# Optimization experiments

Hardware: AMD Instinct MI355X
Metric: run time of the kernel (lower is better)

Reference implementation:

```python
import jax, jax.numpy as jnp
import numpy as np

MEM_HEAD = 4
K_DIM = 256
HALF = K_DIM // 2          # 128
SUB_SIZE = 512
MEM_SIZE = SUB_SIZE * SUB_SIZE  # 262144
KNN = 32
HIDDEN = 512
BN_EPS = 1e-5


def setup_inputs() -> dict:
    key = jax.random.key(0)
    ks = jax.random.split(key, 9)
    B = 4096
    x = jax.random.normal(ks[0], (B, HIDDEN), jnp.float32)
    W1 = jax.random.normal(ks[1], (HIDDEN // 2, HIDDEN), jnp.float32) * (1.0 / np.sqrt(HIDDEN))
    b1 = jnp.zeros((HIDDEN // 2,), jnp.float32)
    W2 = jax.random.normal(ks[2], (2 * HIDDEN, HIDDEN // 2), jnp.float32) * (1.0 / np.sqrt(HIDDEN // 2))
    b2 = jnp.zeros((2 * HIDDEN,), jnp.float32)
    gamma = jnp.ones((2 * HIDDEN,), jnp.float32)
    beta = jnp.zeros((2 * HIDDEN,), jnp.float32)
    # product keys: (heads, 2 halves, n_sub_keys, half_dim), gaussian init
    keys = jax.random.normal(ks[3], (MEM_HEAD, 2, SUB_SIZE, HALF), jnp.float32)
    # EmbeddingBag value table, init std = HIDDEN^-0.5
    values = jax.random.normal(ks[4], (MEM_SIZE, HIDDEN), jnp.float32) * (HIDDEN ** -0.5)
    return dict(x=x, W1=W1, b1=b1, W2=W2, b2=b2, gamma=gamma, beta=beta, keys=keys, values=values)


def reference(x, W1, b1, W2, b2, gamma, beta, keys, values):
    B = x.shape[0]
    # QueryMLP: Linear -> ELU -> Linear -> BatchNorm1d (training-mode batch stats)
    h = jax.nn.elu(x @ W1.T + b1)
    h = h @ W2.T + b2                                  # (B, 2H)
    mu = h.mean(axis=0)
    var = h.var(axis=0)                                # biased, as torch BN
    h = (h - mu) * jax.lax.rsqrt(var + BN_EPS) * gamma + beta
    q = h.reshape(B, MEM_HEAD, K_DIM)                  # (B, heads, k_dim)
    q1, q2 = q[..., :HALF], q[..., HALF:]
    # sub-key scoring per head half
    s1 = jnp.einsum('bhd,hkd->bhk', q1, keys[:, 0])    # (B, heads, SUB_SIZE)
    s2 = jnp.einsum('bhd,hkd->bhk', q2, keys[:, 1])
    t1, i1 = jax.lax.top_k(s1, KNN)                    # (B, heads, KNN)
    t2, i2 = jax.lax.top_k(s2, KNN)
    # cartesian product of the two knn sets
    all_s = (t1[..., :, None] + t2[..., None, :]).reshape(B, MEM_HEAD, KNN * KNN)
    all_i = (i1[..., :, None] * SUB_SIZE + i2[..., None, :]).reshape(B, MEM_HEAD, KNN * KNN)
    sc, best = jax.lax.top_k(all_s, KNN)               # (B, heads, KNN)
    idx = jnp.take_along_axis(all_i, best, axis=-1)
    # softmax over KNN per (sample, head), as in the torch code (dim=-1 on (bs*head, KNN))
    w = jax.nn.softmax(sc, axis=-1).reshape(B, MEM_HEAD * KNN)
    idx = idx.reshape(B, MEM_HEAD * KNN)
    # weighted EmbeddingBag sum
    rows = values[idx]                                 # (B, heads*KNN, HIDDEN)
    out = jnp.einsum('bk,bkd->bd', w, rows)            # (B, HIDDEN)
    return out
```

## Files before the change

kernel.cpp:

```cpp
#include <hip/hip_runtime.h>
#include <math.h>

#define NROWS 4096
#define HIDN  512
#define H1N   256
#define H2N   1024
#define NHEAD 4
#define KDIM  256
#define HALFD 128
#define SUBS  512
#define KNN   32

typedef _Float16 f16x8 __attribute__((ext_vector_type(8)));
typedef _Float16 f16x4v __attribute__((ext_vector_type(4)));
typedef float f32x4  __attribute__((ext_vector_type(4)));

template<int C>
__device__ __forceinline__ unsigned dpp_umax(unsigned x) {
    unsigned m = (unsigned)__builtin_amdgcn_update_dpp((int)x, (int)x, C, 0xf, 0xf, false);
    return x > m ? x : m;
}
__device__ __forceinline__ unsigned wave_umax_bcast(unsigned x) {
    x = dpp_umax<0x111>(x);
    x = dpp_umax<0x112>(x);
    x = dpp_umax<0x114>(x);
    x = dpp_umax<0x118>(x);
    x = dpp_umax<0x142>(x);
    x = dpp_umax<0x143>(x);
    return (unsigned)__builtin_amdgcn_readlane((int)x, 63);
}
template<int C>
__device__ __forceinline__ float dpp_fadd(float x) {
    int m = __builtin_amdgcn_update_dpp(0, __float_as_int(x), C, 0xf, 0xf, true);
    return x + __int_as_float(m);
}
__device__ __forceinline__ float wave_fsum_bcast(float x) {
    x = dpp_fadd<0x111>(x);
    x = dpp_fadd<0x112>(x);
    x = dpp_fadd<0x114>(x);
    x = dpp_fadd<0x118>(x);
    x = dpp_fadd<0x142>(x);
    x = dpp_fadd<0x143>(x);
    return __int_as_float(__builtin_amdgcn_readlane(__float_as_int(x), 63));
}

template<int IB>
__device__ __forceinline__ unsigned pack_key(float v, int j) {
    unsigned b = __float_as_uint(v);
    unsigned x = (unsigned)((int)b >> 31) | 0x80000000u;
    unsigned k = b ^ x;
    constexpr unsigned LM = (1u << IB) - 1u;
    return (k & ~LM) | (LM - (unsigned)j);
}
template<int IB>
__device__ __forceinline__ float dec_key(unsigned k) {
    constexpr unsigned LM = (1u << IB) - 1u;
    unsigned kv = k & ~LM;
    unsigned x = (~(unsigned)((int)kv >> 31)) | 0x80000000u;
    return __uint_as_float(kv ^ x);
}

__device__ __forceinline__ void slot_to_ij(int s, int& io, int& jo) {
    constexpr int O[32] = {0,32,48,58,66,72,77,81,85,88,91,93,95,97,99,101,
                           103,104,105,106,107,108,109,110,111,112,113,114,115,116,117,118};
    int ii = 0, oo = 0;
    #pragma unroll
    for (int k = 1; k < 32; ++k) {
        bool ge = (s >= O[k]);
        ii += ge ? 1 : 0;
        oo = ge ? O[k] : oo;
    }
    io = ii; jo = s - oo;
}

__global__ __launch_bounds__(256)
void cvt_f16(const float* __restrict__ in, _Float16* __restrict__ out)
{
    int i = (blockIdx.x * 256 + threadIdx.x) * 4;
    float4 v = *(const float4*)&in[i];
    f16x4v o = {(_Float16)v.x, (_Float16)v.y, (_Float16)v.z, (_Float16)v.w};
    *(f16x4v*)&out[i] = o;
}

template<int BN, int ACT>
__global__ __launch_bounds__(256)
void gemm_f16(const _Float16* __restrict__ A, const _Float16* __restrict__ B,
              const float* __restrict__ bias, _Float16* __restrict__ C,
              int K, int lda, int ldb, int ldc)
{
    constexpr int WR = (BN == 128) ? 2 : 4;
    constexpr int WM = 128 / WR;
    constexpr int MT = WM / 16;
    constexpr int NT = 4;

    __shared__ _Float16 As[128 * 64];
    __shared__ _Float16 Bs[BN * 64];

    const int t    = threadIdx.x;
    const int m0   = blockIdx.x * 128, n0 = blockIdx.y * BN;
    const int lane = t & 63, wv = t >> 6;
    const int wr   = (BN == 128) ? (wv >> 1) : wv;
    const int wc   = (BN == 128) ? (wv & 1) : 0;
    const int sr   = t >> 3;
    const int sce  = (t & 7) * 8;
    const int swz  = sce * 2;

    const f32x4 fz = {0.f, 0.f, 0.f, 0.f};
    f32x4 acc[MT][NT];
    #pragma unroll
    for (int mt = 0; mt < MT; ++mt)
        #pragma unroll
        for (int nt = 0; nt < NT; ++nt) acc[mt][nt] = fz;

    for (int kb = 0; kb < K; kb += 64) {
        #pragma unroll
        for (int i = 0; i < 4; ++i) {
            int r = sr + 32 * i;
            uint4 v = *(const uint4*)&A[(size_t)(m0 + r) * lda + kb + sce];
            *(uint4*)((char*)As + r * 128 + (swz ^ ((r & 7) << 4))) = v;
        }
        #pragma unroll
        for (int i = 0; i < BN / 32; ++i) {
            int r = sr + 32 * i;
            uint4 v = *(const uint4*)&B[(size_t)(n0 + r) * ldb + kb + sce];
            *(uint4*)((char*)Bs + r * 128 + (swz ^ ((r & 7) << 4))) = v;
        }
        __syncthreads();
        #pragma unroll
        for (int ks = 0; ks < 2; ++ks) {
            const int kbyte = ks * 64 + (lane >> 4) * 16;
            f16x8 ah[MT], bf[NT];
            #pragma unroll
            for (int mt = 0; mt < MT; ++mt) {
                int r = wr * WM + mt * 16 + (lane & 15);
                ah[mt] = *(const f16x8*)((const char*)As + r * 128 + (kbyte ^ ((r & 7) << 4)));
            }
            #pragma unroll
            for (int nt = 0; nt < NT; ++nt) {
                int r = wc * 64 + nt * 16 + (lane & 15);
                bf[nt] = *(const f16x8*)((const char*)Bs + r * 128 + (kbyte ^ ((r & 7) << 4)));
            }
            #pragma unroll
            for (int mt = 0; mt < MT; ++mt)
                #pragma unroll
                for (int nt = 0; nt < NT; ++nt)
                    acc[mt][nt] = __builtin_amdgcn_mfma_f32_16x16x32_f16(ah[mt], bf[nt], acc[mt][nt], 0, 0, 0);
        }
        __syncthreads();
    }

    #pragma unroll
    for (int mt = 0; mt < MT; ++mt) {
        #pragma unroll
        for (int nt = 0; nt < NT; ++nt) {
            int col = n0 + wc * 64 + nt * 16 + (lane & 15);
            float bz = bias[col];
            #pragma unroll
            for (int j = 0; j < 4; ++j) {
                int row = m0 + wr * WM + mt * 16 + (lane >> 4) * 4 + j;
                float v = acc[mt][nt][j] + bz;
                if (ACT) v = v > 0.f ? v : expm1f(v);
                C[(size_t)row * ldc + col] = (_Float16)v;
            }
        }
    }
}

__global__ __launch_bounds__(256)
void bn_partial_h(const _Float16* __restrict__ h2f, float* __restrict__ part)
{
    int col = blockIdx.x * 256 + threadIdx.x;
    int r0  = blockIdx.y * 256;
    float s = 0.f, q = 0.f;
    for (int rr = r0; rr < r0 + 256; ++rr) {
        float v = (float)h2f[(size_t)rr * H2N + col];
        s += v; q += v * v;
    }
    part[(size_t)blockIdx.y * H2N + col] = s;
    part[(size_t)16 * H2N + (size_t)blockIdx.y * H2N + col] = q;
}

__global__ __launch_bounds__(256)
void bn_finalize(const float* __restrict__ part, const float* __restrict__ gamma,
                 const float* __restrict__ beta, float* __restrict__ scale,
                 float* __restrict__ shift)
{
    int col = blockIdx.x * 256 + threadIdx.x;
    float s = 0.f, q = 0.f;
    for (int c = 0; c < 16; ++c) {
        s += part[(size_t)c * H2N + col];
        q += part[(size_t)16 * H2N + (size_t)c * H2N + col];
    }
    float mu  = s * (1.f / NROWS);
    float var = q * (1.f / NROWS) - mu * mu;
    float sc  = gamma[col] / sqrtf(var + 1e-5f);
    scale[col] = sc;
    shift[col] = beta[col] - mu * sc;
}

__global__ __launch_bounds__(256)
void keys_prep(const float* __restrict__ keys, const float* __restrict__ scale,
               const float* __restrict__ shift, _Float16* __restrict__ keysp,
               float* __restrict__ biasp)
{
    const int gid  = blockIdx.x * 4 + (threadIdx.x >> 6);
    const int lane = threadIdx.x & 63;
    const int z    = gid >> 9;
    const float* krow = keys + (size_t)gid * HALFD;
    const int d0 = lane * 2;
    float k0 = krow[d0], k1 = krow[d0 + 1];
    float sc0 = scale[z * HALFD + d0], sc1 = scale[z * HALFD + d0 + 1];
    float sh0 = shift[z * HALFD + d0], sh1 = shift[z * HALFD + d0 + 1];
    _Float16 p0 = (_Float16)(sc0 * k0), p1 = (_Float16)(sc1 * k1);
    unsigned u;
    {
        union { _Float16 h[2]; unsigned u; } cvt;
        cvt.h[0] = p0; cvt.h[1] = p1;
        u = cvt.u;
    }
    *(unsigned*)&keysp[(size_t)gid * HALFD + d0] = u;
    float dot = wave_fsum_bcast(k0 * sh0 + k1 * sh1);
    if (lane == 0) biasp[gid] = dot;
}

__global__ __launch_bounds__(256)
void score_f16(const _Float16* __restrict__ h2f, const _Float16* __restrict__ keysp,
               const float* __restrict__ biasp, float* __restrict__ s1, float* __restrict__ s2)
{
    __shared__ _Float16 As[128 * 64];
    __shared__ _Float16 Bs[128 * 64];

    const int t    = threadIdx.x;
    const int z    = blockIdx.z;
    const int m0   = blockIdx.x * 128, n0 = blockIdx.y * 128;
    const int lane = t & 63, wv = t >> 6;
    const int wr   = wv >> 1, wc = wv & 1;
    const int sr   = t >> 3;
    const int sce  = (t & 7) * 8;
    const int swz  = sce * 2;

    const _Float16* A = h2f + z * HALFD;
    const _Float16* B = keysp + (size_t)z * SUBS * HALFD;
    float* outb = (z & 1) ? s2 : s1;
    const int hd = z >> 1;

    const f32x4 fz = {0.f, 0.f, 0.f, 0.f};
    f32x4 acc[4][4];
    #pragma unroll
    for (int mt = 0; mt < 4; ++mt)
        #pragma unroll
        for (int nt = 0; nt < 4; ++nt) acc[mt][nt] = fz;

    for (int kb = 0; kb < HALFD; kb += 64) {
        #pragma unroll
        for (int i = 0; i < 4; ++i) {
            int r = sr + 32 * i;
            uint4 v = *(const uint4*)&A[(size_t)(m0 + r) * H2N + kb + sce];
            *(uint4*)((char*)As + r * 128 + (swz ^ ((r & 7) << 4))) = v;
        }
        #pragma unroll
        for (int i = 0; i < 4; ++i) {
            int r = sr + 32 * i;
            uint4 v = *(const uint4*)&B[(size_t)(n0 + r) * HALFD + kb + sce];
            *(uint4*)((char*)Bs + r * 128 + (swz ^ ((r & 7) << 4))) = v;
        }
        __syncthreads();
        #pragma unroll
        for (int ks = 0; ks < 2; ++ks) {
            const int kbyte = ks * 64 + (lane >> 4) * 16;
            f16x8 af[4], bf[4];
            #pragma unroll
            for (int mt = 0; mt < 4; ++mt) {
                int r = wr * 64 + mt * 16 + (lane & 15);
                af[mt] = *(const f16x8*)((const char*)As + r * 128 + (kbyte ^ ((r & 7) << 4)));
            }
            #pragma unroll
            for (int nt = 0; nt < 4; ++nt) {
                int r = wc * 64 + nt * 16 + (lane & 15);
                bf[nt] = *(const f16x8*)((const char*)Bs + r * 128 + (kbyte ^ ((r & 7) << 4)));
            }
            #pragma unroll
            for (int mt = 0; mt < 4; ++mt)
                #pragma unroll
                for (int nt = 0; nt < 4; ++nt)
                    acc[mt][nt] = __builtin_amdgcn_mfma_f32_16x16x32_f16(af[mt], bf[nt], acc[mt][nt], 0, 0, 0);
        }
        __syncthreads();
    }

    #pragma unroll
    for (int mt = 0; mt < 4; ++mt) {
        #pragma unroll
        for (int nt = 0; nt < 4; ++nt) {
            int col = n0 + wc * 64 + nt * 16 + (lane & 15);
            float bz = biasp[z * SUBS + col];
            #pragma unroll
            for (int j = 0; j < 4; ++j) {
                int row = m0 + wr * 64 + mt * 16 + (lane >> 4) * 4 + j;
                outb[((size_t)row * NHEAD + hd) * SUBS + col] = acc[mt][nt][j] + bz;
            }
        }
    }
}

__global__ __launch_bounds__(512)
void topk_gather(const float* __restrict__ s1, const float* __restrict__ s2,
                 const float* __restrict__ values, float* __restrict__ out)
{
    const int b    = blockIdx.x;
    const int t    = threadIdx.x;
    const int w    = t >> 6;
    const int lane = t & 63;

    __shared__ unsigned Ksh[8][KNN];
    __shared__ float wgt_sh[NHEAD * KNN];
    __shared__ int   idx_sh[NHEAD * KNN];
    __shared__ float4 pacc[4][128];

    {
        const int head = w >> 1, half = w & 1;
        const float* srow = (half ? s2 : s1) + ((size_t)b * NHEAD + head) * SUBS;
        float4 va = ((const float4*)srow)[lane * 2];
        float4 vb = ((const float4*)srow)[lane * 2 + 1];
        const int j0 = lane * 8;
        unsigned k0 = pack_key<9>(va.x, j0+0), k1 = pack_key<9>(va.y, j0+1);
        unsigned k2 = pack_key<9>(va.z, j0+2), k3 = pack_key<9>(va.w, j0+3);
        unsigned k4 = pack_key<9>(vb.x, j0+4), k5 = pack_key<9>(vb.y, j0+5);
        unsigned k6 = pack_key<9>(vb.z, j0+6), k7 = pack_key<9>(vb.w, j0+7);

        #define CEU(a,b) { unsigned _mx = (a)>(b)?(a):(b); unsigned _mn = (a)>(b)?(b):(a); (a)=_mx; (b)=_mn; }
        CEU(k0,k1) CEU(k2,k3) CEU(k4,k5) CEU(k6,k7)
        CEU(k0,k2) CEU(k1,k3) CEU(k4,k6) CEU(k5,k7)
        CEU(k1,k2) CEU(k5,k6)
        CEU(k0,k4) CEU(k1,k5) CEU(k2,k6) CEU(k3,k7)
        CEU(k2,k4) CEU(k3,k5)
        CEU(k1,k2) CEU(k3,k4) CEU(k5,k6)
        #undef CEU

        unsigned kk = 0;
        #pragma unroll
        for (int rr = 0; rr < KNN; ++rr) {
            unsigned bv = wave_umax_bcast(k0);
            bool win = (k0 == bv);
            k0 = win ? k1 : k0;
            k1 = win ? k2 : k1;
            k2 = win ? k3 : k2;
            k3 = win ? k4 : k3;
            k4 = win ? k5 : k4;
            k5 = win ? k6 : k5;
            k6 = win ? k7 : k6;
            k7 = win ? 0u : k7;
            kk = (lane == rr) ? bv : kk;
        }
        if (lane < KNN) Ksh[w][lane] = kk;
    }
    __syncthreads();

    if (w < NHEAD) {
        const int h = w;
        const unsigned* T1 = Ksh[2*h];
        const unsigned* T2 = Ksh[2*h+1];

        unsigned c0 = 0, c1 = 0;
        {
            int ia, ja;
            slot_to_ij(lane, ia, ja);
            if (lane < 119) {
                float s = dec_key<9>(T1[ia]) + dec_key<9>(T2[ja]);
                c0 = pack_key<7>(s, lane);
            }
            if (lane + 64 < 119) {
                int ib2, jb2;
                slot_to_ij(lane + 64, ib2, jb2);
                float s = dec_key<9>(T1[ib2]) + dec_key<9>(T2[jb2]);
                c1 = pack_key<7>(s, lane + 64);
            }
        }

        unsigned kk = 0;
        #pragma unroll
        for (int rr = 0; rr < KNN; ++rr) {
            unsigned m  = c0 > c1 ? c0 : c1;
            unsigned bv = wave_umax_bcast(m);
            bool f0 = (c0 == bv);
            bool f1 = (c1 == bv);
            c0 = f0 ? 0u : c0;
            c1 = f1 ? 0u : c1;
            kk = (lane == rr) ? bv : kk;
        }

        unsigned mk = (unsigned)__builtin_amdgcn_readlane((int)kk, 0);
        float mx = dec_key<7>(mk);
        float sv = dec_key<7>(kk);
        float e  = (lane < KNN) ? __expf(sv - mx) : 0.f;
        float Z  = wave_fsum_bcast(e);

        if (lane < KNN) {
            int slot = 127 - (int)(kk & 127u);
            int i, j;
            slot_to_ij(slot, i, j);
            int i1 = 511 - (int)(T1[i] & 511u);
            int i2 = 511 - (int)(T2[j] & 511u);
            wgt_sh[h * KNN + lane] = e / Z;
            idx_sh[h * KNN + lane] = i1 * SUBS + i2;
        }
    }
    __syncthreads();

    const int sub = t >> 7;
    const int c4  = t & 127;
    #define EADDR(i) ((const float4*)(values + (size_t)idx_sh[((i)<<2)|sub] * HIDN) + c4)
    float4 b0 = *EADDR(0), b1 = *EADDR(1), b2 = *EADDR(2), b3 = *EADDR(3);
    float4 b4 = *EADDR(4), b5 = *EADDR(5), b6 = *EADDR(6), b7 = *EADDR(7);
    float4 a0 = make_float4(0.f,0.f,0.f,0.f);
    float4 a1 = make_float4(0.f,0.f,0.f,0.f);
    #define FMA4(acc, wg, v) { acc.x = fmaf(wg, v.x, acc.x); acc.y = fmaf(wg, v.y, acc.y); \
                               acc.z = fmaf(wg, v.z, acc.z); acc.w = fmaf(wg, v.w, acc.w); }
    #define STEPR(bi, ei, acc) { float wg = wgt_sh[((ei)<<2)|sub]; FMA4(acc, wg, bi); bi = *EADDR((ei)+8); }
    #define STEPN(bi, ei, acc) { float wg = wgt_sh[((ei)<<2)|sub]; FMA4(acc, wg, bi); }
    STEPR(b0, 0, a0) STEPR(b1, 1, a1) STEPR(b2, 2, a0) STEPR(b3, 3, a1)
    STEPR(b4, 4, a0) STEPR(b5, 5, a1) STEPR(b6, 6, a0) STEPR(b7, 7, a1)
    STEPR(b0, 8, a0) STEPR(b1, 9, a1) STEPR(b2,10, a0) STEPR(b3,11, a1)
    STEPR(b4,12, a0) STEPR(b5,13, a1) STEPR(b6,14, a0) STEPR(b7,15, a1)
    STEPR(b0,16, a0) STEPR(b1,17, a1) STEPR(b2,18, a0) STEPR(b3,19, a1)
    STEPR(b4,20, a0) STEPR(b5,21, a1) STEPR(b6,22, a0) STEPR(b7,23, a1)
    STEPN(b0,24, a0) STEPN(b1,25, a1) STEPN(b2,26, a0) STEPN(b3,27, a1)
    STEPN(b4,28, a0) STEPN(b5,29, a1) STEPN(b6,30, a0) STEPN(b7,31, a1)
    #undef STEPR
    #undef STEPN
    #undef FMA4
    #undef EADDR
    float4 acc;
    acc.x = a0.x + a1.x; acc.y = a0.y + a1.y;
    acc.z = a0.z + a1.z; acc.w = a0.w + a1.w;

    pacc[sub][c4] = acc;
    __syncthreads();
    if (t < 128) {
        float4 r0 = pacc[0][t], r1 = pacc[1][t], r2 = pacc[2][t], r3 = pacc[3][t];
        float4 r;
        r.x = (r0.x + r1.x) + (r2.x + r3.x);
        r.y = (r0.y + r1.y) + (r2.y + r3.y);
        r.z = (r0.z + r1.z) + (r2.z + r3.z);
        r.w = (r0.w + r1.w) + (r2.w + r3.w);
        ((float4*)(out + (size_t)b * HIDN))[t] = r;
    }
}

extern "C" void kernel_launch(void* const* d_in, const int* in_sizes, int n_in,
                              void* d_out, int out_size, void* d_ws, size_t ws_size,
                              hipStream_t stream)
{
    const float* x      = (const float*)d_in[0];
    const float* W1     = (const float*)d_in[1];
    const float* b1     = (const float*)d_in[2];
    const float* W2     = (const float*)d_in[3];
    const float* b2     = (const float*)d_in[4];
    const float* gamma  = (const float*)d_in[5];
    const float* beta   = (const float*)d_in[6];
    const float* keys   = (const float*)d_in[7];
    const float* values = (const float*)d_in[8];
    float* out = (float*)d_out;

    float* ws    = (float*)d_ws;
    float* part  = ws;
    float* scale = part + (size_t)32 * H2N;
    float* shift = scale + H2N;
    float* s1    = shift + H2N;
    float* s2    = s1 + (size_t)NROWS * NHEAD * SUBS;
    float* biasp = s2 + (size_t)NROWS * NHEAD * SUBS;
    _Float16* xh    = (_Float16*)(biasp + 4096);
    _Float16* w1h   = xh  + (size_t)NROWS * HIDN;
    _Float16* w2h   = w1h + (size_t)H1N * HIDN;
    _Float16* h1h   = w2h + (size_t)H2N * H1N;
    _Float16* h2f   = h1h + (size_t)NROWS * H1N;
    _Float16* keysp = h2f + (size_t)NROWS * H2N;

    cvt_f16<<<dim3((NROWS * HIDN) / 1024), 256, 0, stream>>>(x, xh);
    cvt_f16<<<dim3((H1N * HIDN) / 1024), 256, 0, stream>>>(W1, w1h);
    cvt_f16<<<dim3((H2N * H1N) / 1024), 256, 0, stream>>>(W2, w2h);

    gemm_f16<64, 1><<<dim3(NROWS/128, H1N/64), 256, 0, stream>>>(
        xh, w1h, b1, h1h, HIDN, HIDN, HIDN, H1N);
    gemm_f16<128, 0><<<dim3(NROWS/128, H2N/128), 256, 0, stream>>>(
        h1h, w2h, b2, h2f, H1N, H1N, H1N, H2N);

    bn_partial_h<<<dim3(H2N/256, 16), 256, 0, stream>>>(h2f, part);
    bn_finalize<<<dim3(H2N/256), 256, 0, stream>>>(part, gamma, beta, scale, shift);

    keys_prep<<<dim3(1024), 256, 0, stream>>>(keys, scale, shift, keysp, biasp);

    score_f16<<<dim3(NROWS/128, SUBS/128, NHEAD*2), 256, 0, stream>>>(h2f, keysp, biasp, s1, s2);

    topk_gather<<<dim3(NROWS), 512, 0, stream>>>(s1, s2, values, out);
}
```

Baseline: 235.5 us.

## Fuse sub-key top-k into score GEMM, keeping full score rows in LDS

The score GEMM now computes a full 64x512 score tile per block (all sub-keys for one head half) and packs the biased scores into sortable keys in shared memory. It then runs the per-row top-32 selection in the same kernel and writes only the packed top-k keys to global memory. This removes the write and re-read of the two full 4096x4x512 fp32 score tensors. In exchange it uses about 128 KB of LDS per block, which lowers occupancy, and the selection now runs serially over 8 rows per wave.

```diff
diff --git a/kernel.cpp b/kernel.cpp
--- a/kernel.cpp
+++ b/kernel.cpp
@@ -223,110 +223,88 @@
     if (lane == 0) biasp[gid] = dot;
 }
 
-__global__ __launch_bounds__(256)
-void score_f16(const _Float16* __restrict__ h2f, const _Float16* __restrict__ keysp,
-               const float* __restrict__ biasp, float* __restrict__ s1, float* __restrict__ s2)
-{
-    __shared__ _Float16 As[128 * 64];
-    __shared__ _Float16 Bs[128 * 64];
+__global__ __launch_bounds__(512)
+void score_topk(const _Float16* __restrict__ h2f, const _Float16* __restrict__ keysp,
+                const float* __restrict__ biasp, unsigned* __restrict__ t_all)
+{
+    __shared__ unsigned smem[64 * 513];
+    _Float16* As = (_Float16*)smem;
+    _Float16* Bs = (_Float16*)smem + 4096;
 
     const int t    = threadIdx.x;
-    const int z    = blockIdx.z;
-    const int m0   = blockIdx.x * 128, n0 = blockIdx.y * 128;
+    const int z    = blockIdx.y;
+    const int m0   = blockIdx.x * 64;
     const int lane = t & 63, wv = t >> 6;
-    const int wr   = wv >> 1, wc = wv & 1;
+    const int wr   = wv >> 2, wc = wv & 3;
     const int sr   = t >> 3;
     const int sce  = (t & 7) * 8;
     const int swz  = sce * 2;
 
     const _Float16* A = h2f + z * HALFD;
     const _Float16* B = keysp + (size_t)z * SUBS * HALFD;
-    float* outb = (z & 1) ? s2 : s1;
-    const int hd = z >> 1;
 
     const f32x4 fz = {0.f, 0.f, 0.f, 0.f};
-    f32x4 acc[4][4];
+    f32x4 acc[2][8];
     #pragma unroll
-    for (int mt = 0; mt < 4; ++mt)
-        #pragma unroll
-        for (int nt = 0; nt < 4; ++nt) acc[mt][nt] = fz;
+    for (int mt = 0; mt < 2; ++mt)
+        #pragma unroll
+        for (int nt = 0; nt < 8; ++nt) acc[mt][nt] = fz;
 
     for (int kb = 0; kb < HALFD; kb += 64) {
-        #pragma unroll
-        for (int i = 0; i < 4; ++i) {
-            int r = sr + 32 * i;
-            uint4 v = *(const uint4*)&A[(size_t)(m0 + r) * H2N + kb + sce];
-            *(uint4*)((char*)As + r * 128 + (swz ^ ((r & 7) << 4))) = v;
-        }
-        #pragma unroll
-        for (int i = 0; i < 4; ++i) {
-            int r = sr + 32 * i;
-            uint4 v = *(const uint4*)&B[(size_t)(n0 + r) * HALFD + kb + sce];
+        {
+            uint4 v = *(const uint4*)&A[(size_t)(m0 + sr) * H2N + kb + sce];
+            *(uint4*)((char*)As + sr * 128 + (swz ^ ((sr & 7) << 4))) = v;
+        }
+        #pragma unroll
+        for (int i = 0; i < 8; ++i) {
+            int r = sr + 64 * i;
+            uint4 v = *(const uint4*)&B[(size_t)r * HALFD + kb + sce];
             *(uint4*)((char*)Bs + r * 128 + (swz ^ ((r & 7) << 4))) = v;
         }
         __syncthreads();
         #pragma unroll
         for (int ks = 0; ks < 2; ++ks) {
             const int kbyte = ks * 64 + (lane >> 4) * 16;
-            f16x8 af[4], bf[4];
-            #pragma unroll
-            for (int mt = 0; mt < 4; ++mt) {
-                int r = wr * 64 + mt * 16 + (lane & 15);
+            f16x8 af[2], bf[8];
+            #pragma unroll
+            for (int mt = 0; mt < 2; ++mt) {
+                int r = wr * 32 + mt * 16 + (lane & 15);
                 af[mt] = *(const f16x8*)((const char*)As + r * 128 + (kbyte ^ ((r & 7) << 4)));
             }
             #pragma unroll
-            for (int nt = 0; nt < 4; ++nt) {
-                int r = wc * 64 + nt * 16 + (lane & 15);
+            for (int nt = 0; nt < 8; ++nt) {
+                int r = wc * 128 + nt * 16 + (lane & 15);
                 bf[nt] = *(const f16x8*)((const char*)Bs + r * 128 + (kbyte ^ ((r & 7) << 4)));
             }
             #pragma unroll
-            for (int mt = 0; mt < 4; ++mt)
+            for (int mt = 0; mt < 2; ++mt)
                 #pragma unroll
-                for (int nt = 0; nt < 4; ++nt)
+                for (int nt = 0; nt < 8; ++nt)
                     acc[mt][nt] = __builtin_amdgcn_mfma_f32_16x16x32_f16(af[mt], bf[nt], acc[mt][nt], 0, 0, 0);
         }
         __syncthreads();
     }
 
     #pragma unroll
-    for (int mt = 0; mt < 4; ++mt) {
-        #pragma unroll
-        for (int nt = 0; nt < 4; ++nt) {
-            int col = n0 + wc * 64 + nt * 16 + (lane & 15);
+    for (int mt = 0; mt < 2; ++mt) {
+        #pragma unroll
+        for (int nt = 0; nt < 8; ++nt) {
+            int col = wc * 128 + nt * 16 + (lane & 15);
             float bz = biasp[z * SUBS + col];
             #pragma unroll
             for (int j = 0; j < 4; ++j) {
-                int row = m0 + wr * 64 + mt * 16 + (lane >> 4) * 4 + j;
-                outb[((size_t)row * NHEAD + hd) * SUBS + col] = acc[mt][nt][j] + bz;
-            }
-        }
-    }
-}
-
-__global__ __launch_bounds__(512)
-void topk_gather(const float* __restrict__ s1, const float* __restrict__ s2,
-                 const float* __restrict__ values, float* __restrict__ out)
-{
-    const int b    = blockIdx.x;
-    const int t    = threadIdx.x;
-    const int w    = t >> 6;
-    const int lane = t & 63;
-
-    __shared__ unsigned Ksh[8][KNN];
-    __shared__ float wgt_sh[NHEAD * KNN];
-    __shared__ int   idx_sh[NHEAD * KNN];
-    __shared__ float4 pacc[4][128];
-
-    {
-        const int head = w >> 1, half = w & 1;
-        const float* srow = (half ? s2 : s1) + ((size_t)b * NHEAD + head) * SUBS;
-        float4 va = ((const float4*)srow)[lane * 2];
-        float4 vb = ((const float4*)srow)[lane * 2 + 1];
-        const int j0 = lane * 8;
-        unsigned k0 = pack_key<9>(va.x, j0+0), k1 = pack_key<9>(va.y, j0+1);
-        unsigned k2 = pack_key<9>(va.z, j0+2), k3 = pack_key<9>(va.w, j0+3);
-        unsigned k4 = pack_key<9>(vb.x, j0+4), k5 = pack_key<9>(vb.y, j0+5);
-        unsigned k6 = pack_key<9>(vb.z, j0+6), k7 = pack_key<9>(vb.w, j0+7);
+                int row = wr * 32 + mt * 16 + (lane >> 4) * 4 + j;
+                smem[row * 513 + col] = pack_key<9>(acc[mt][nt][j] + bz, col);
+            }
+        }
+    }
+    __syncthreads();
+
+    for (int rr8 = 0; rr8 < 8; ++rr8) {
+        const int r = wv * 8 + rr8;
+        const unsigned* rowp = &smem[r * 513 + lane * 8];
+        unsigned k0 = rowp[0], k1 = rowp[1], k2 = rowp[2], k3 = rowp[3];
+        unsigned k4 = rowp[4], k5 = rowp[5], k6 = rowp[6], k7 = rowp[7];
 
         #define CEU(a,b) { unsigned _mx = (a)>(b)?(a):(b); unsigned _mn = (a)>(b)?(b):(a); (a)=_mx; (b)=_mn; }
         CEU(k0,k1) CEU(k2,k3) CEU(k4,k5) CEU(k6,k7)
@@ -352,8 +330,26 @@
             k7 = win ? 0u : k7;
             kk = (lane == rr) ? bv : kk;
         }
-        if (lane < KNN) Ksh[w][lane] = kk;
-    }
+        if (lane < KNN)
+            t_all[((size_t)(m0 + r) * 8 + z) * KNN + lane] = kk;
+    }
+}
+
+__global__ __launch_bounds__(512)
+void topk_gather(const unsigned* __restrict__ t_all,
+                 const float* __restrict__ values, float* __restrict__ out)
+{
+    const int b    = blockIdx.x;
+    const int t    = threadIdx.x;
+    const int w    = t >> 6;
+    const int lane = t & 63;
+
+    __shared__ unsigned Ksh[8][KNN];
+    __shared__ float wgt_sh[NHEAD * KNN];
+    __shared__ int   idx_sh[NHEAD * KNN];
+    __shared__ float4 pacc[4][128];
+
+    if (lane < KNN) Ksh[w][lane] = t_all[((size_t)b * 8 + w) * KNN + lane];
     __syncthreads();
 
     if (w < NHEAD) {
@@ -466,10 +462,9 @@
     float* part  = ws;
     float* scale = part + (size_t)32 * H2N;
     float* shift = scale + H2N;
-    float* s1    = shift + H2N;
-    float* s2    = s1 + (size_t)NROWS * NHEAD * SUBS;
-    float* biasp = s2 + (size_t)NROWS * NHEAD * SUBS;
-    _Float16* xh    = (_Float16*)(biasp + 4096);
+    float* biasp = shift + H2N;
+    unsigned* t_all = (unsigned*)(biasp + 4096);
+    _Float16* xh    = (_Float16*)(t_all + (size_t)NROWS * 8 * KNN);
     _Float16* w1h   = xh  + (size_t)NROWS * HIDN;
     _Float16* w2h   = w1h + (size_t)H1N * HIDN;
     _Float16* h1h   = w2h + (size_t)H2N * H1N;
@@ -490,7 +485,7 @@
 
     keys_prep<<<dim3(1024), 256, 0, stream>>>(keys, scale, shift, keysp, biasp);
 
-    score_f16<<<dim3(NROWS/128, SUBS/128, NHEAD*2), 256, 0, stream>>>(h2f, keysp, biasp, s1, s2);
-
-    topk_gather<<<dim3(NROWS), 512, 0, stream>>>(s1, s2, values, out);
-}
+    score_topk<<<dim3(NROWS/64, 8), 512, 0, stream>>>(h2f, keysp, biasp, t_all);
+
+    topk_gather<<<dim3(NROWS), 512, 0, stream>>>(t_all, values, out);
+}
```

After: 269.6 us. 14.4% more time.
